# Kernel optimization log

Hardware: AMD Instinct MI355X
Metric: run time of the kernel (lower is better)

Reference implementation:

```python
import jax, jax.numpy as jnp
import numpy as np

N_NODES, N_EDGES, DIM, N_LAYERS, N_GRAPHS, N_CLASSES = 50000, 640000, 128, 5, 512, 128


def setup_inputs() -> dict:
    key = jax.random.key(0)
    ks = jax.random.split(key, 10)
    x = jnp.zeros((N_NODES,), dtype=jnp.int32)  # Embedding(1, D) -> all indices 0
    edge_index = jax.random.randint(ks[0], (2, N_EDGES), 0, N_NODES, dtype=jnp.int32)
    edge_attr = jax.random.normal(ks[1], (N_EDGES, DIM), dtype=jnp.float32)
    batch = jnp.sort(jax.random.randint(ks[2], (N_NODES,), 0, N_GRAPHS, dtype=jnp.int32))
    s = 1.0 / np.sqrt(DIM)
    node_emb = jax.random.normal(ks[3], (1, DIM), dtype=jnp.float32)
    Ws = jax.random.normal(ks[4], (N_LAYERS, DIM, DIM), dtype=jnp.float32) * s
    bs = jnp.zeros((N_LAYERS, DIM), dtype=jnp.float32)
    Wes = jax.random.normal(ks[5], (N_LAYERS, DIM, DIM), dtype=jnp.float32) * s
    Wp = jax.random.normal(ks[6], (DIM, N_CLASSES), dtype=jnp.float32) * s
    bp = jnp.zeros((N_CLASSES,), dtype=jnp.float32)
    return {"x": x, "edge_index": edge_index, "edge_attr": edge_attr, "batch": batch,
            "node_emb": node_emb, "Ws": Ws, "bs": bs, "Wes": Wes, "Wp": Wp, "bp": bp}


def reference(x, edge_index, edge_attr, batch, node_emb, Ws, bs, Wes, Wp, bp):
    src, dst = edge_index[0], edge_index[1]
    h = node_emb[x]  # [N, D] embedding lookup (vocab=1)
    n = h.shape[0]
    e = src.shape[0]
    deg = jax.ops.segment_sum(jnp.ones((e,), h.dtype), dst, num_segments=n)
    deg = jnp.maximum(deg, 1.0)[:, None]  # mean aggregation denominator
    for l in range(N_LAYERS):
        hw = h @ Ws[l] + bs[l]                       # [N, D]
        msg = hw[src] + edge_attr @ Wes[l]           # [E, D] gather + edge transform
        agg = jax.ops.segment_sum(msg, dst, num_segments=n) / deg  # scatter-mean
        h = agg + hw                                 # root connection
        if l < N_LAYERS - 1:
            h = jax.nn.relu(h)                       # relu on all but last layer
        # dropout is identity in eval mode
    g = N_GRAPHS
    cnt = jnp.maximum(jax.ops.segment_sum(jnp.ones((n,), h.dtype), batch, num_segments=g), 1.0)
    pooled = jax.ops.segment_sum(h, batch, num_segments=g) / cnt[:, None]  # global_mean_pool
    return pooled @ Wp + bp  # [G, num_clases]
```

## Files before the change

kernel.cpp:

```cpp
#include <hip/hip_runtime.h>

#define N_NODES   50000
#define N_EDGES   640000
#define DIM       128
#define N_LAYERS  5
#define N_GRAPHS  512
#define N_CLASSES 128
#define NB_SCAN   196

typedef __attribute__((ext_vector_type(8))) short short8;
typedef __attribute__((ext_vector_type(4))) float floatx4;

__device__ inline float bfhi(unsigned u) { return __uint_as_float(u & 0xffff0000u); }
__device__ inline float bflo(unsigned u) { return __uint_as_float(u << 16); }
__device__ inline unsigned f2bf(float f) {
  unsigned x = __float_as_uint(f);
  return (x + 0x7fffu + ((x >> 16) & 1u)) >> 16;
}

__global__ void k_zero(int* __restrict__ deg, int* __restrict__ fill,
                       float* __restrict__ pool, float* __restrict__ cnt) {
  int i = blockIdx.x * 256 + threadIdx.x;
  if (i < N_NODES) { deg[i] = 0; fill[i] = 0; }
  if (i < N_GRAPHS * DIM) pool[i] = 0.f;
  if (i < N_GRAPHS) cnt[i] = 0.f;
}

__global__ void k_deg(const int* __restrict__ dst, int* __restrict__ deg) {
  int e = blockIdx.x * 256 + threadIdx.x;
  if (e < N_EDGES) atomicAdd(&deg[dst[e]], 1);
}

__global__ void k_scan1(const int* __restrict__ deg, int* __restrict__ bsum) {
  __shared__ int s[256];
  int t = threadIdx.x, i = blockIdx.x * 256 + t;
  s[t] = (i < N_NODES) ? deg[i] : 0;
  __syncthreads();
  for (int o = 128; o > 0; o >>= 1) {
    if (t < o) s[t] += s[t + o];
    __syncthreads();
  }
  if (t == 0) bsum[blockIdx.x] = s[0];
}

__global__ void k_scan2(int* __restrict__ bsum) {
  __shared__ int s[256];
  int t = threadIdx.x;
  s[t] = (t < NB_SCAN) ? bsum[t] : 0;
  __syncthreads();
  for (int o = 1; o < 256; o <<= 1) {
    int add = (t >= o) ? s[t - o] : 0;
    __syncthreads();
    s[t] += add;
    __syncthreads();
  }
  int ex = (t == 0) ? 0 : s[t - 1];
  if (t < NB_SCAN) bsum[t] = ex;
}

__global__ void k_scan3(const int* __restrict__ deg, const int* __restrict__ bsum,
                        int* __restrict__ row_ptr) {
  __shared__ int s[256];
  int t = threadIdx.x, i = blockIdx.x * 256 + t;
  s[t] = (i < N_NODES) ? deg[i] : 0;
  __syncthreads();
  for (int o = 1; o < 256; o <<= 1) {
    int add = (t >= o) ? s[t - o] : 0;
    __syncthreads();
    s[t] += add;
    __syncthreads();
  }
  int ex = bsum[blockIdx.x] + ((t == 0) ? 0 : s[t - 1]);
  if (i < N_NODES) row_ptr[i] = ex;
  if (blockIdx.x == 0 && t == 0) row_ptr[N_NODES] = N_EDGES;
}

__global__ void k_fill(const int* __restrict__ src, const int* __restrict__ dst,
                       const int* __restrict__ row_ptr, int* __restrict__ fill,
                       int* __restrict__ col_src, int* __restrict__ col_eid) {
  int e = blockIdx.x * 256 + threadIdx.x;
  if (e < N_EDGES) {
    int d = dst[e];
    int pos = row_ptr[d] + atomicAdd(&fill[d], 1);
    col_src[pos] = src[e];
    col_eid[pos] = e;
  }
}

__global__ void k_wconv(const float* __restrict__ Ws, const float* __restrict__ Wes,
                        unsigned short* __restrict__ Wt_s, unsigned short* __restrict__ Wt_e) {
  int idx = blockIdx.x * 256 + threadIdx.x;
  int which = idx / (N_LAYERS * DIM * DIM);
  int rem = idx - which * (N_LAYERS * DIM * DIM);
  int l = rem >> 14;
  int c = (rem >> 7) & 127;
  int k = rem & 127;
  const float* W = which ? Wes : Ws;
  unsigned short* O = which ? Wt_e : Wt_s;
  float v = W[((size_t)l * DIM + k) * DIM + c];
  O[((size_t)l * DIM + c) * DIM + k] = (unsigned short)f2bf(v);
}

__global__ void k_ean_init(const int* __restrict__ row_ptr, const int* __restrict__ col_eid,
                           const float* __restrict__ edge_attr, const int* __restrict__ x,
                           const float* __restrict__ node_emb,
                           unsigned short* __restrict__ ean, float* __restrict__ rdeg,
                           unsigned short* __restrict__ h) {
  int sub = threadIdx.x >> 5;
  int lane = threadIdx.x & 31;
  int i = blockIdx.x * 8 + sub;
  if (i >= N_NODES) return;
  int b = row_ptr[i], e = row_ptr[i + 1];
  float4 acc = make_float4(0.f, 0.f, 0.f, 0.f);
  for (int p = b; p < e; p++) {
    int eid = col_eid[p];
    float4 v = ((const float4*)(edge_attr + (size_t)eid * DIM))[lane];
    acc.x += v.x; acc.y += v.y; acc.z += v.z; acc.w += v.w;
  }
  float r = 1.0f / (float)max(e - b, 1);
  if (lane == 0) rdeg[i] = r;
  uint2 o;
  o.x = f2bf(acc.x * r) | (f2bf(acc.y * r) << 16);
  o.y = f2bf(acc.z * r) | (f2bf(acc.w * r) << 16);
  ((uint2*)(ean + (size_t)i * DIM))[lane] = o;
  float4 hv = ((const float4*)(node_emb + (size_t)x[i] * DIM))[lane];
  uint2 ho;
  ho.x = f2bf(hv.x) | (f2bf(hv.y) << 16);
  ho.y = f2bf(hv.z) | (f2bf(hv.w) << 16);
  ((uint2*)(h + (size_t)i * DIM))[lane] = ho;
}

__global__ void k_gather(const int* __restrict__ row_ptr, const int* __restrict__ col_src,
                         const unsigned short* __restrict__ h, const float* __restrict__ rdeg,
                         unsigned short* __restrict__ u) {
  int sub = threadIdx.x >> 4;
  int lane = threadIdx.x & 15;
  int i = blockIdx.x * 16 + sub;
  if (i >= N_NODES) return;
  int b = row_ptr[i], e = row_ptr[i + 1];
  float a0 = 0.f, a1 = 0.f, a2 = 0.f, a3 = 0.f, a4 = 0.f, a5 = 0.f, a6 = 0.f, a7 = 0.f;
  for (int p = b; p < e; p++) {
    int j = col_src[p];
    uint4 v = *(const uint4*)(h + (size_t)j * DIM + lane * 8);
    a0 += bflo(v.x); a1 += bfhi(v.x);
    a2 += bflo(v.y); a3 += bfhi(v.y);
    a4 += bflo(v.z); a5 += bfhi(v.z);
    a6 += bflo(v.w); a7 += bfhi(v.w);
  }
  float r = rdeg[i];
  uint4 hv = *(const uint4*)(h + (size_t)i * DIM + lane * 8);
  uint4 o;
  o.x = f2bf(bflo(hv.x) + a0 * r) | (f2bf(bfhi(hv.x) + a1 * r) << 16);
  o.y = f2bf(bflo(hv.y) + a2 * r) | (f2bf(bfhi(hv.y) + a3 * r) << 16);
  o.z = f2bf(bflo(hv.z) + a4 * r) | (f2bf(bfhi(hv.z) + a5 * r) << 16);
  o.w = f2bf(bflo(hv.w) + a6 * r) | (f2bf(bfhi(hv.w) + a7 * r) << 16);
  *(uint4*)(u + (size_t)i * DIM + lane * 8) = o;
}

__global__ __launch_bounds__(256) void k_gemm(
    const unsigned short* __restrict__ A0, const unsigned short* __restrict__ A1,
    const unsigned short* __restrict__ W0, const unsigned short* __restrict__ W1,
    const float* __restrict__ bias, unsigned short* __restrict__ hout, int relu) {
  __shared__ unsigned short sA[64][72];
  __shared__ unsigned short sW[128][72];
  int tid = threadIdx.x;
  int wave = tid >> 6, lane = tid & 63;
  int quad = lane >> 4, l16 = lane & 15;
  int row0 = blockIdx.x * 64;
  floatx4 acc[8];
  #pragma unroll
  for (int ci = 0; ci < 8; ci++) acc[ci] = (floatx4){0.f, 0.f, 0.f, 0.f};

  for (int m = 0; m < 2; m++) {
    const unsigned short* A = m ? A1 : A0;
    const unsigned short* W = m ? W1 : W0;
    for (int kc = 0; kc < 128; kc += 64) {
      __syncthreads();
      #pragma unroll
      for (int q = 0; q < 2; q++) {
        int s = tid + 256 * q;
        int r = s >> 3, seg = s & 7;
        int grow = row0 + r;
        uint4 v = make_uint4(0u, 0u, 0u, 0u);
        if (grow < N_NODES)
          v = *(const uint4*)(A + (size_t)grow * DIM + kc + seg * 8);
        *(uint4*)(&sA[r][seg * 8]) = v;
      }
      #pragma unroll
      for (int q = 0; q < 4; q++) {
        int s = tid + 256 * q;
        int r = s >> 3, seg = s & 7;
        *(uint4*)(&sW[r][seg * 8]) =
            *(const uint4*)(W + (size_t)r * DIM + kc + seg * 8);
      }
      __syncthreads();
      #pragma unroll
      for (int ks = 0; ks < 64; ks += 32) {
        short8 a = *(const short8*)(&sA[wave * 16 + l16][ks + quad * 8]);
        #pragma unroll
        for (int ci = 0; ci < 8; ci++) {
          short8 b = *(const short8*)(&sW[ci * 16 + l16][ks + quad * 8]);
          acc[ci] = __builtin_amdgcn_mfma_f32_16x16x32_bf16(a, b, acc[ci], 0, 0, 0);
        }
      }
    }
  }
  #pragma unroll
  for (int ci = 0; ci < 8; ci++) {
    int col = ci * 16 + l16;
    float bv = bias[col];
    #pragma unroll
    for (int r = 0; r < 4; r++) {
      int row = row0 + wave * 16 + quad * 4 + r;
      if (row < N_NODES) {
        float v = acc[ci][r] + bv;
        if (relu) v = fmaxf(v, 0.f);
        hout[(size_t)row * DIM + col] = (unsigned short)f2bf(v);
      }
    }
  }
}

__global__ void k_pool(const unsigned short* __restrict__ h, const int* __restrict__ batch,
                       float* __restrict__ pool, float* __restrict__ cnt) {
  int t = threadIdx.x;
  int i0 = blockIdx.x * 128;
  int iend = min(i0 + 128, N_NODES);
  float acc = 0.f;
  int cur = -1, run = 0;
  for (int i = i0; i < iend; i++) {
    int g = batch[i];
    if (g != cur) {
      if (cur >= 0) {
        atomicAdd(&pool[(size_t)cur * DIM + t], acc);
        if (t == 0) atomicAdd(&cnt[cur], (float)run);
      }
      acc = 0.f; run = 0; cur = g;
    }
    acc += __uint_as_float(((unsigned)h[(size_t)i * DIM + t]) << 16);
    run++;
  }
  if (cur >= 0) {
    atomicAdd(&pool[(size_t)cur * DIM + t], acc);
    if (t == 0) atomicAdd(&cnt[cur], (float)run);
  }
}

__global__ void k_out(const float* __restrict__ pool, const float* __restrict__ cnt,
                      const float* __restrict__ Wp, const float* __restrict__ bp,
                      float* __restrict__ out) {
  __shared__ float sp[DIM];
  int g = blockIdx.x, t = threadIdx.x;
  sp[t] = pool[(size_t)g * DIM + t];
  __syncthreads();
  float r = 1.0f / fmaxf(cnt[g], 1.0f);
  float acc = 0.f;
  for (int k = 0; k < DIM; k++) acc += sp[k] * Wp[(size_t)k * N_CLASSES + t];
  out[(size_t)g * N_CLASSES + t] = acc * r + bp[t];
}

extern "C" void kernel_launch(void* const* d_in, const int* in_sizes, int n_in,
                              void* d_out, int out_size, void* d_ws, size_t ws_size,
                              hipStream_t stream) {
  (void)in_sizes; (void)n_in; (void)out_size; (void)ws_size;
  const int*   x          = (const int*)d_in[0];
  const int*   edge_index = (const int*)d_in[1];
  const float* edge_attr  = (const float*)d_in[2];
  const int*   batch      = (const int*)d_in[3];
  const float* node_emb   = (const float*)d_in[4];
  const float* Ws         = (const float*)d_in[5];
  const float* bs         = (const float*)d_in[6];
  const float* Wes        = (const float*)d_in[7];
  const float* Wp         = (const float*)d_in[8];
  const float* bp         = (const float*)d_in[9];
  float* out = (float*)d_out;
  const int* src = edge_index;
  const int* dst = edge_index + N_EDGES;

  char* p = (char*)d_ws;
  auto alloc = [&](size_t bytes) {
    void* q = (void*)p;
    p += (bytes + 255) & ~(size_t)255;
    return q;
  };
  unsigned short* h    = (unsigned short*)alloc((size_t)N_NODES * DIM * 2);
  unsigned short* u    = (unsigned short*)alloc((size_t)N_NODES * DIM * 2);
  unsigned short* ean  = (unsigned short*)alloc((size_t)N_NODES * DIM * 2);
  unsigned short* Wt_s = (unsigned short*)alloc((size_t)N_LAYERS * DIM * DIM * 2);
  unsigned short* Wt_e = (unsigned short*)alloc((size_t)N_LAYERS * DIM * DIM * 2);
  int*   deg     = (int*)  alloc((size_t)N_NODES * 4);
  float* rdeg    = (float*)alloc((size_t)N_NODES * 4);
  int*   row_ptr = (int*)  alloc((size_t)(N_NODES + 64) * 4);
  int*   fill    = (int*)  alloc((size_t)N_NODES * 4);
  int*   col_src = (int*)  alloc((size_t)N_EDGES * 4);
  int*   col_eid = (int*)  alloc((size_t)N_EDGES * 4);
  float* pool    = (float*)alloc((size_t)N_GRAPHS * DIM * 4);
  float* cnt     = (float*)alloc((size_t)N_GRAPHS * 4);
  int*   bsum    = (int*)  alloc(256 * 4);

  k_zero<<<256, 256, 0, stream>>>(deg, fill, pool, cnt);
  k_deg<<<(N_EDGES + 255) / 256, 256, 0, stream>>>(dst, deg);
  k_scan1<<<NB_SCAN, 256, 0, stream>>>(deg, bsum);
  k_scan2<<<1, 256, 0, stream>>>(bsum);
  k_scan3<<<NB_SCAN, 256, 0, stream>>>(deg, bsum, row_ptr);
  k_fill<<<(N_EDGES + 255) / 256, 256, 0, stream>>>(src, dst, row_ptr, fill, col_src, col_eid);
  k_wconv<<<(2 * N_LAYERS * DIM * DIM) / 256, 256, 0, stream>>>(Ws, Wes, Wt_s, Wt_e);
  k_ean_init<<<(N_NODES + 7) / 8, 256, 0, stream>>>(row_ptr, col_eid, edge_attr, x,
                                                    node_emb, ean, rdeg, h);
  for (int l = 0; l < N_LAYERS; l++) {
    k_gather<<<(N_NODES + 15) / 16, 256, 0, stream>>>(row_ptr, col_src, h, rdeg, u);
    k_gemm<<<(N_NODES + 63) / 64, 256, 0, stream>>>(
        u, ean, Wt_s + (size_t)l * DIM * DIM, Wt_e + (size_t)l * DIM * DIM,
        bs + (size_t)l * DIM, h, (l < N_LAYERS - 1) ? 1 : 0);
  }
  k_pool<<<(N_NODES + 127) / 128, 128, 0, stream>>>(h, batch, pool, cnt);
  k_out<<<N_GRAPHS, N_CLASSES, 0, stream>>>(pool, cnt, Wp, bp, out);
}
```

Before: 871.0 us.

## Fuse neighbor gather into layer GEMM and fold first layer algebraically

Each layer's neighbor mean-gather now happens inside the GEMM kernel, writing into shared memory instead of a global intermediate. That removes one kernel launch per layer and the round-trip of the u buffer through memory. Because all nodes share the single embedding, layer 0 collapses to a per-column vector (node_emb@Ws0), scaled by whether the node has in-edges, plus the edge-attribute term. This skips the first gather entirely. Source and edge ids are packed into one int2 CSR array, and the gather loops are unrolled. The price is larger shared-memory use per block (lower occupancy) and a dependence on the vocabulary-1 embedding structure.

```diff
diff --git a/kernel.cpp b/kernel.cpp
--- a/kernel.cpp
+++ b/kernel.cpp
@@ -77,13 +77,12 @@
 
 __global__ void k_fill(const int* __restrict__ src, const int* __restrict__ dst,
                        const int* __restrict__ row_ptr, int* __restrict__ fill,
-                       int* __restrict__ col_src, int* __restrict__ col_eid) {
+                       int2* __restrict__ col) {
   int e = blockIdx.x * 256 + threadIdx.x;
   if (e < N_EDGES) {
     int d = dst[e];
     int pos = row_ptr[d] + atomicAdd(&fill[d], 1);
-    col_src[pos] = src[e];
-    col_eid[pos] = e;
+    col[pos] = make_int2(src[e], e);
   }
 }
 
@@ -101,66 +100,47 @@
   O[((size_t)l * DIM + c) * DIM + k] = (unsigned short)f2bf(v);
 }
 
-__global__ void k_ean_init(const int* __restrict__ row_ptr, const int* __restrict__ col_eid,
-                           const float* __restrict__ edge_attr, const int* __restrict__ x,
-                           const float* __restrict__ node_emb,
-                           unsigned short* __restrict__ ean, float* __restrict__ rdeg,
-                           unsigned short* __restrict__ h) {
+__global__ void k_v0(const float* __restrict__ node_emb, const float* __restrict__ Ws0,
+                     float* __restrict__ v0) {
+  int c = threadIdx.x;
+  float acc = 0.f;
+  for (int k = 0; k < DIM; k++) acc += node_emb[k] * Ws0[(size_t)k * DIM + c];
+  v0[c] = acc;
+}
+
+__global__ void k_ean_init(const int* __restrict__ row_ptr, const int2* __restrict__ col,
+                           const float* __restrict__ edge_attr,
+                           unsigned short* __restrict__ ean, float* __restrict__ rdeg) {
   int sub = threadIdx.x >> 5;
   int lane = threadIdx.x & 31;
   int i = blockIdx.x * 8 + sub;
   if (i >= N_NODES) return;
   int b = row_ptr[i], e = row_ptr[i + 1];
-  float4 acc = make_float4(0.f, 0.f, 0.f, 0.f);
-  for (int p = b; p < e; p++) {
-    int eid = col_eid[p];
-    float4 v = ((const float4*)(edge_attr + (size_t)eid * DIM))[lane];
-    acc.x += v.x; acc.y += v.y; acc.z += v.z; acc.w += v.w;
+  float ax = 0.f, ay = 0.f, az = 0.f, aw = 0.f;
+  int p = b;
+  for (; p + 2 <= e; p += 2) {
+    int e0 = col[p].y, e1 = col[p + 1].y;
+    float4 v0 = ((const float4*)(edge_attr + (size_t)e0 * DIM))[lane];
+    float4 v1 = ((const float4*)(edge_attr + (size_t)e1 * DIM))[lane];
+    ax += v0.x + v1.x; ay += v0.y + v1.y; az += v0.z + v1.z; aw += v0.w + v1.w;
+  }
+  if (p < e) {
+    int e0 = col[p].y;
+    float4 v0 = ((const float4*)(edge_attr + (size_t)e0 * DIM))[lane];
+    ax += v0.x; ay += v0.y; az += v0.z; aw += v0.w;
   }
   float r = 1.0f / (float)max(e - b, 1);
   if (lane == 0) rdeg[i] = r;
   uint2 o;
-  o.x = f2bf(acc.x * r) | (f2bf(acc.y * r) << 16);
-  o.y = f2bf(acc.z * r) | (f2bf(acc.w * r) << 16);
+  o.x = f2bf(ax * r) | (f2bf(ay * r) << 16);
+  o.y = f2bf(az * r) | (f2bf(aw * r) << 16);
   ((uint2*)(ean + (size_t)i * DIM))[lane] = o;
-  float4 hv = ((const float4*)(node_emb + (size_t)x[i] * DIM))[lane];
-  uint2 ho;
-  ho.x = f2bf(hv.x) | (f2bf(hv.y) << 16);
-  ho.y = f2bf(hv.z) | (f2bf(hv.w) << 16);
-  ((uint2*)(h + (size_t)i * DIM))[lane] = ho;
-}
-
-__global__ void k_gather(const int* __restrict__ row_ptr, const int* __restrict__ col_src,
-                         const unsigned short* __restrict__ h, const float* __restrict__ rdeg,
-                         unsigned short* __restrict__ u) {
-  int sub = threadIdx.x >> 4;
-  int lane = threadIdx.x & 15;
-  int i = blockIdx.x * 16 + sub;
-  if (i >= N_NODES) return;
-  int b = row_ptr[i], e = row_ptr[i + 1];
-  float a0 = 0.f, a1 = 0.f, a2 = 0.f, a3 = 0.f, a4 = 0.f, a5 = 0.f, a6 = 0.f, a7 = 0.f;
-  for (int p = b; p < e; p++) {
-    int j = col_src[p];
-    uint4 v = *(const uint4*)(h + (size_t)j * DIM + lane * 8);
-    a0 += bflo(v.x); a1 += bfhi(v.x);
-    a2 += bflo(v.y); a3 += bfhi(v.y);
-    a4 += bflo(v.z); a5 += bfhi(v.z);
-    a6 += bflo(v.w); a7 += bfhi(v.w);
-  }
-  float r = rdeg[i];
-  uint4 hv = *(const uint4*)(h + (size_t)i * DIM + lane * 8);
-  uint4 o;
-  o.x = f2bf(bflo(hv.x) + a0 * r) | (f2bf(bfhi(hv.x) + a1 * r) << 16);
-  o.y = f2bf(bflo(hv.y) + a2 * r) | (f2bf(bfhi(hv.y) + a3 * r) << 16);
-  o.z = f2bf(bflo(hv.z) + a4 * r) | (f2bf(bfhi(hv.z) + a5 * r) << 16);
-  o.w = f2bf(bflo(hv.w) + a6 * r) | (f2bf(bfhi(hv.w) + a7 * r) << 16);
-  *(uint4*)(u + (size_t)i * DIM + lane * 8) = o;
-}
-
-__global__ __launch_bounds__(256) void k_gemm(
-    const unsigned short* __restrict__ A0, const unsigned short* __restrict__ A1,
-    const unsigned short* __restrict__ W0, const unsigned short* __restrict__ W1,
-    const float* __restrict__ bias, unsigned short* __restrict__ hout, int relu) {
+}
+
+__global__ __launch_bounds__(256) void k_gemm0(
+    const unsigned short* __restrict__ ean, const unsigned short* __restrict__ W1,
+    const float* __restrict__ v0, const float* __restrict__ bias,
+    const int* __restrict__ deg, unsigned short* __restrict__ hout) {
   __shared__ unsigned short sA[64][72];
   __shared__ unsigned short sW[128][72];
   int tid = threadIdx.x;
@@ -171,21 +151,126 @@
   #pragma unroll
   for (int ci = 0; ci < 8; ci++) acc[ci] = (floatx4){0.f, 0.f, 0.f, 0.f};
 
+  for (int kc = 0; kc < 128; kc += 64) {
+    __syncthreads();
+    #pragma unroll
+    for (int q = 0; q < 2; q++) {
+      int s = tid + 256 * q;
+      int r = s >> 3, seg = s & 7;
+      int grow = row0 + r;
+      uint4 v = make_uint4(0u, 0u, 0u, 0u);
+      if (grow < N_NODES)
+        v = *(const uint4*)(ean + (size_t)grow * DIM + kc + seg * 8);
+      *(uint4*)(&sA[r][seg * 8]) = v;
+    }
+    #pragma unroll
+    for (int q = 0; q < 4; q++) {
+      int s = tid + 256 * q;
+      int r = s >> 3, seg = s & 7;
+      *(uint4*)(&sW[r][seg * 8]) =
+          *(const uint4*)(W1 + (size_t)r * DIM + kc + seg * 8);
+    }
+    __syncthreads();
+    #pragma unroll
+    for (int ks = 0; ks < 64; ks += 32) {
+      short8 a = *(const short8*)(&sA[wave * 16 + l16][ks + quad * 8]);
+      #pragma unroll
+      for (int ci = 0; ci < 8; ci++) {
+        short8 b = *(const short8*)(&sW[ci * 16 + l16][ks + quad * 8]);
+        acc[ci] = __builtin_amdgcn_mfma_f32_16x16x32_bf16(a, b, acc[ci], 0, 0, 0);
+      }
+    }
+  }
+  #pragma unroll
+  for (int ci = 0; ci < 8; ci++) {
+    int col = ci * 16 + l16;
+    float bv = bias[col];
+    float vv = v0[col];
+    #pragma unroll
+    for (int r = 0; r < 4; r++) {
+      int row = row0 + wave * 16 + quad * 4 + r;
+      if (row < N_NODES) {
+        float s = (deg[row] > 0) ? 2.f : 1.f;
+        float v = acc[ci][r] + bv + s * vv;
+        v = fmaxf(v, 0.f);
+        hout[(size_t)row * DIM + col] = (unsigned short)f2bf(v);
+      }
+    }
+  }
+}
+
+#define ACC8(v) { a0 += bflo(v.x); a1 += bfhi(v.x); a2 += bflo(v.y); a3 += bfhi(v.y); \
+                  a4 += bflo(v.z); a5 += bfhi(v.z); a6 += bflo(v.w); a7 += bfhi(v.w); }
+
+__global__ __launch_bounds__(256) void k_layer(
+    const int* __restrict__ row_ptr, const int2* __restrict__ col,
+    const unsigned short* __restrict__ hin, const float* __restrict__ rdeg,
+    const unsigned short* __restrict__ ean,
+    const unsigned short* __restrict__ W0, const unsigned short* __restrict__ W1,
+    const float* __restrict__ bias, unsigned short* __restrict__ hout, int relu) {
+  __shared__ unsigned short sU[64][136];
+  __shared__ unsigned short sE[64][136];
+  __shared__ unsigned short sW[128][72];
+  int tid = threadIdx.x;
+  int row0 = blockIdx.x * 64;
+
+  #pragma unroll
+  for (int q = 0; q < 4; q++) {
+    int s = tid + 256 * q;
+    int r = s >> 4, seg = s & 15;
+    int grow = row0 + r;
+    uint4 v = make_uint4(0u, 0u, 0u, 0u);
+    if (grow < N_NODES) v = *(const uint4*)(ean + (size_t)grow * DIM + seg * 8);
+    *(uint4*)(&sE[r][seg * 8]) = v;
+  }
+
+  {
+    int g = tid >> 4, lane = tid & 15;
+    for (int n = 0; n < 4; n++) {
+      int r = g + n * 16;
+      int i = row0 + r;
+      if (i < N_NODES) {
+        int b = row_ptr[i], e = row_ptr[i + 1];
+        float a0 = 0.f, a1 = 0.f, a2 = 0.f, a3 = 0.f,
+              a4 = 0.f, a5 = 0.f, a6 = 0.f, a7 = 0.f;
+        int p = b;
+        for (; p + 4 <= e; p += 4) {
+          int j0 = col[p].x, j1 = col[p + 1].x, j2 = col[p + 2].x, j3 = col[p + 3].x;
+          uint4 v0 = *(const uint4*)(hin + (size_t)j0 * DIM + lane * 8);
+          uint4 v1 = *(const uint4*)(hin + (size_t)j1 * DIM + lane * 8);
+          uint4 v2 = *(const uint4*)(hin + (size_t)j2 * DIM + lane * 8);
+          uint4 v3 = *(const uint4*)(hin + (size_t)j3 * DIM + lane * 8);
+          ACC8(v0); ACC8(v1); ACC8(v2); ACC8(v3);
+        }
+        for (; p < e; p++) {
+          int j0 = col[p].x;
+          uint4 v0 = *(const uint4*)(hin + (size_t)j0 * DIM + lane * 8);
+          ACC8(v0);
+        }
+        float rr = rdeg[i];
+        uint4 hv = *(const uint4*)(hin + (size_t)i * DIM + lane * 8);
+        uint4 o;
+        o.x = f2bf(bflo(hv.x) + a0 * rr) | (f2bf(bfhi(hv.x) + a1 * rr) << 16);
+        o.y = f2bf(bflo(hv.y) + a2 * rr) | (f2bf(bfhi(hv.y) + a3 * rr) << 16);
+        o.z = f2bf(bflo(hv.z) + a4 * rr) | (f2bf(bfhi(hv.z) + a5 * rr) << 16);
+        o.w = f2bf(bflo(hv.w) + a6 * rr) | (f2bf(bfhi(hv.w) + a7 * rr) << 16);
+        *(uint4*)(&sU[r][lane * 8]) = o;
+      } else {
+        *(uint4*)(&sU[r][lane * 8]) = make_uint4(0u, 0u, 0u, 0u);
+      }
+    }
+  }
+
+  int wave = tid >> 6, lane = tid & 63;
+  int quad = lane >> 4, l16 = lane & 15;
+  floatx4 acc[8];
+  #pragma unroll
+  for (int ci = 0; ci < 8; ci++) acc[ci] = (floatx4){0.f, 0.f, 0.f, 0.f};
+
   for (int m = 0; m < 2; m++) {
-    const unsigned short* A = m ? A1 : A0;
     const unsigned short* W = m ? W1 : W0;
     for (int kc = 0; kc < 128; kc += 64) {
       __syncthreads();
-      #pragma unroll
-      for (int q = 0; q < 2; q++) {
-        int s = tid + 256 * q;
-        int r = s >> 3, seg = s & 7;
-        int grow = row0 + r;
-        uint4 v = make_uint4(0u, 0u, 0u, 0u);
-        if (grow < N_NODES)
-          v = *(const uint4*)(A + (size_t)grow * DIM + kc + seg * 8);
-        *(uint4*)(&sA[r][seg * 8]) = v;
-      }
       #pragma unroll
       for (int q = 0; q < 4; q++) {
         int s = tid + 256 * q;
@@ -196,7 +281,8 @@
       __syncthreads();
       #pragma unroll
       for (int ks = 0; ks < 64; ks += 32) {
-        short8 a = *(const short8*)(&sA[wave * 16 + l16][ks + quad * 8]);
+        short8 a = m ? *(const short8*)(&sE[wave * 16 + l16][kc + ks + quad * 8])
+                     : *(const short8*)(&sU[wave * 16 + l16][kc + ks + quad * 8]);
         #pragma unroll
         for (int ci = 0; ci < 8; ci++) {
           short8 b = *(const short8*)(&sW[ci * 16 + l16][ks + quad * 8]);
@@ -207,15 +293,15 @@
   }
   #pragma unroll
   for (int ci = 0; ci < 8; ci++) {
-    int col = ci * 16 + l16;
-    float bv = bias[col];
+    int col_ = ci * 16 + l16;
+    float bv = bias[col_];
     #pragma unroll
     for (int r = 0; r < 4; r++) {
       int row = row0 + wave * 16 + quad * 4 + r;
       if (row < N_NODES) {
         float v = acc[ci][r] + bv;
         if (relu) v = fmaxf(v, 0.f);
-        hout[(size_t)row * DIM + col] = (unsigned short)f2bf(v);
+        hout[(size_t)row * DIM + col_] = (unsigned short)f2bf(v);
       }
     }
   }
@@ -273,6 +359,7 @@
   const float* Wes        = (const float*)d_in[7];
   const float* Wp         = (const float*)d_in[8];
   const float* bp         = (const float*)d_in[9];
+  (void)x;
   float* out = (float*)d_out;
   const int* src = edge_index;
   const int* dst = edge_index + N_EDGES;
@@ -284,7 +371,7 @@
     return q;
   };
   unsigned short* h    = (unsigned short*)alloc((size_t)N_NODES * DIM * 2);
-  unsigned short* u    = (unsigned short*)alloc((size_t)N_NODES * DIM * 2);
+  unsigned short* h2   = (unsigned short*)alloc((size_t)N_NODES * DIM * 2);
   unsigned short* ean  = (unsigned short*)alloc((size_t)N_NODES * DIM * 2);
   unsigned short* Wt_s = (unsigned short*)alloc((size_t)N_LAYERS * DIM * DIM * 2);
   unsigned short* Wt_e = (unsigned short*)alloc((size_t)N_LAYERS * DIM * DIM * 2);
@@ -292,26 +379,32 @@
   float* rdeg    = (float*)alloc((size_t)N_NODES * 4);
   int*   row_ptr = (int*)  alloc((size_t)(N_NODES + 64) * 4);
   int*   fill    = (int*)  alloc((size_t)N_NODES * 4);
-  int*   col_src = (int*)  alloc((size_t)N_EDGES * 4);
-  int*   col_eid = (int*)  alloc((size_t)N_EDGES * 4);
+  int2*  col     = (int2*) alloc((size_t)N_EDGES * 8);
   float* pool    = (float*)alloc((size_t)N_GRAPHS * DIM * 4);
   float* cnt     = (float*)alloc((size_t)N_GRAPHS * 4);
   int*   bsum    = (int*)  alloc(256 * 4);
+  float* v0      = (float*)alloc(DIM * 4);
 
   k_zero<<<256, 256, 0, stream>>>(deg, fill, pool, cnt);
   k_deg<<<(N_EDGES + 255) / 256, 256, 0, stream>>>(dst, deg);
   k_scan1<<<NB_SCAN, 256, 0, stream>>>(deg, bsum);
   k_scan2<<<1, 256, 0, stream>>>(bsum);
   k_scan3<<<NB_SCAN, 256, 0, stream>>>(deg, bsum, row_ptr);
-  k_fill<<<(N_EDGES + 255) / 256, 256, 0, stream>>>(src, dst, row_ptr, fill, col_src, col_eid);
+  k_fill<<<(N_EDGES + 255) / 256, 256, 0, stream>>>(src, dst, row_ptr, fill, col);
   k_wconv<<<(2 * N_LAYERS * DIM * DIM) / 256, 256, 0, stream>>>(Ws, Wes, Wt_s, Wt_e);
-  k_ean_init<<<(N_NODES + 7) / 8, 256, 0, stream>>>(row_ptr, col_eid, edge_attr, x,
-                                                    node_emb, ean, rdeg, h);
-  for (int l = 0; l < N_LAYERS; l++) {
-    k_gather<<<(N_NODES + 15) / 16, 256, 0, stream>>>(row_ptr, col_src, h, rdeg, u);
-    k_gemm<<<(N_NODES + 63) / 64, 256, 0, stream>>>(
-        u, ean, Wt_s + (size_t)l * DIM * DIM, Wt_e + (size_t)l * DIM * DIM,
-        bs + (size_t)l * DIM, h, (l < N_LAYERS - 1) ? 1 : 0);
+  k_v0<<<1, DIM, 0, stream>>>(node_emb, Ws, v0);
+  k_ean_init<<<(N_NODES + 7) / 8, 256, 0, stream>>>(row_ptr, col, edge_attr, ean, rdeg);
+
+  k_gemm0<<<(N_NODES + 63) / 64, 256, 0, stream>>>(
+      ean, Wt_e, v0, bs, deg, h);
+  const unsigned short* hin = h;
+  unsigned short* hout = h2;
+  for (int l = 1; l < N_LAYERS; l++) {
+    k_layer<<<(N_NODES + 63) / 64, 256, 0, stream>>>(
+        row_ptr, col, hin, rdeg, ean,
+        Wt_s + (size_t)l * DIM * DIM, Wt_e + (size_t)l * DIM * DIM,
+        bs + (size_t)l * DIM, hout, (l < N_LAYERS - 1) ? 1 : 0);
+    const unsigned short* tmp = hout; hout = (unsigned short*)hin; hin = tmp;
   }
   k_pool<<<(N_NODES + 127) / 128, 128, 0, stream>>>(h, batch, pool, cnt);
   k_out<<<N_GRAPHS, N_CLASSES, 0, stream>>>(pool, cnt, Wp, bp, out);
```

Result: faster. 848.5 us (-2.6%).
